# Performance work log

Measured on AMD Instinct MI355X. Metric: run time of the kernel, lower is better.

Reference implementation:

```python
import jax, jax.numpy as jnp
import numpy as np

NUM_HEADS = 16

def setup_inputs() -> dict:
    key = jax.random.key(0)
    kq, kk, kv = jax.random.split(key, 3)
    B, S, D = 4, 2048, 1024
    return {
        "queries": jax.random.normal(kq, (B, S, D), dtype=jnp.float32),
        "keys": jax.random.normal(kk, (B, S, D), dtype=jnp.float32),
        "values": jax.random.normal(kv, (B, S, D), dtype=jnp.float32),
    }

def _split_heads(x):
    # [B, S, D] -> [B, H, S, Dh]
    B, S, D = x.shape
    return x.reshape(B, S, NUM_HEADS, D // NUM_HEADS).transpose(0, 2, 1, 3)

def reference(queries, keys, values):
    q = _split_heads(queries)   # [B, H, S, Dh]
    k = _split_heads(keys)
    v = _split_heads(values)
    d_k = k.shape[-1]
    scale = 1.0 / jnp.sqrt(jnp.asarray(d_k, dtype=q.dtype))
    # [B, H, S, S] score matrix (materialized, as in the original bmm path)
    scores = jnp.einsum('bhqd,bhkd->bhqk', q, k) * scale
    weights = jax.nn.softmax(scores, axis=-1)
    out = jnp.einsum('bhqk,bhkd->bhqd', weights, v)  # [B, H, S, Dh]
    B, H, S, Dh = out.shape
    return out.transpose(0, 2, 1, 3).reshape(B, S, H * Dh)
```

## Files before the change

kernel.cpp:

```cpp
#include <hip/hip_runtime.h>
#include <hip/hip_bf16.h>
#include <math.h>

#define SEQ    2048
#define NH     16
#define DH     64
#define DMODEL 1024
#define KT     64
#define NT     (SEQ/KT)
#define KH_BYTES (4 * NH * SEQ * DH * 2)

typedef __bf16 bf16x8 __attribute__((ext_vector_type(8)));
typedef float  f32x4  __attribute__((ext_vector_type(4)));
typedef float  f32x16 __attribute__((ext_vector_type(16)));
typedef unsigned u32x2 __attribute__((ext_vector_type(2)));
typedef unsigned short u16x8 __attribute__((ext_vector_type(8)));
typedef __attribute__((address_space(3))) unsigned int        lds_u32_t;
typedef __attribute__((address_space(1))) const unsigned int  g_u32_t;

__device__ __forceinline__ ushort f2bf(float f) {
    union { __hip_bfloat16 h; ushort u; } z;
    z.h = __float2bfloat16(f);
    return z.u;
}

__device__ __forceinline__ unsigned pk2(float lo, float hi) {
    unsigned r;
    asm("v_cvt_pk_bf16_f32 %0, %1, %2" : "=v"(r) : "v"(lo), "v"(hi));
    return r;
}

__device__ __forceinline__ float fexp2(float x) {
#if __has_builtin(__builtin_amdgcn_exp2f)
    return __builtin_amdgcn_exp2f(x);
#else
    float r; asm("v_exp_f32 %0, %1\n\ts_nop 0" : "=v"(r) : "v"(x)); return r;
#endif
}

__device__ __forceinline__ void load16(const char* g, char* l) {
    __builtin_amdgcn_global_load_lds((g_u32_t*)g, (lds_u32_t*)l, 16, 0, 0);
}

__global__ __launch_bounds__(256)
void prep_kv(const float* __restrict__ K, const float* __restrict__ V,
             ushort* __restrict__ Kh, ushort* __restrict__ Vt) {
    __shared__ __attribute__((aligned(16))) unsigned T[64 * 32];
    int blk = blockIdx.x;
    int tid = threadIdx.x;
    int isV = blk >> 11;
    int tix = blk & 2047;
    int st = tix & 31, bh = tix >> 5;
    int b = bh >> 4, h = bh & 15;
    int s0 = st * 64;
    int sr  = tid >> 2;
    int seg = tid & 3;

    const float* ip = (isV ? V : K) + ((size_t)(b * SEQ + s0 + sr)) * DMODEL + h * DH + seg * 16;
    float4 f0 = ((const float4*)ip)[0];
    float4 f1 = ((const float4*)ip)[1];
    float4 f2 = ((const float4*)ip)[2];
    float4 f3 = ((const float4*)ip)[3];
    unsigned wv[8];
    wv[0] = pk2(f0.x, f0.y); wv[1] = pk2(f0.z, f0.w);
    wv[2] = pk2(f1.x, f1.y); wv[3] = pk2(f1.z, f1.w);
    wv[4] = pk2(f2.x, f2.y); wv[5] = pk2(f2.z, f2.w);
    wv[6] = pk2(f3.x, f3.y); wv[7] = pk2(f3.z, f3.w);

    if (!isV) {
        union { unsigned u[4]; u16x8 v; } a, c;
        a.u[0]=wv[0]; a.u[1]=wv[1]; a.u[2]=wv[2]; a.u[3]=wv[3];
        c.u[0]=wv[4]; c.u[1]=wv[5]; c.u[2]=wv[6]; c.u[3]=wv[7];
        ushort* op = Kh + ((size_t)bh * SEQ + s0 + sr) * DH + seg * 16;
        *(u16x8*)op = a.v;
        *(u16x8*)(op + 8) = c.v;
    } else {
        int key = sr & 31;
        #pragma unroll
        for (int j = 0; j < 8; ++j) {
            int pos = (seg * 8 + j) ^ key;
            T[sr * 32 + pos] = wv[j];
        }
        __syncthreads();
        int dr = sr;
        int sseg = seg;
        const char* TB = (const char*)T;
        u16x8 o0, o1;
        #pragma unroll
        for (int i = 0; i < 8; ++i) {
            int s = sseg * 16 + i;
            int off = s * 128 + ((((dr >> 1) ^ (s & 31)) << 2) | ((dr & 1) << 1));
            o0[i] = *(const ushort*)(TB + off);
        }
        #pragma unroll
        for (int i = 0; i < 8; ++i) {
            int s = sseg * 16 + 8 + i;
            int off = s * 128 + ((((dr >> 1) ^ (s & 31)) << 2) | ((dr & 1) << 1));
            o1[i] = *(const ushort*)(TB + off);
        }
        ushort* op = Vt + (size_t)bh * (SEQ * DH) + st * (64 * 64) + dr * 64 + sseg * 16;
        *(u16x8*)op = o0;
        *(u16x8*)(op + 8) = o1;
    }
}

__global__ __launch_bounds__(256, 2)
void mha_fwd32(const float* __restrict__ Q, const ushort* __restrict__ Kh,
               const ushort* __restrict__ Vt, float* __restrict__ Out) {
    int raw = blockIdx.x;
    int bid = (raw & 7) * 64 + (raw >> 3);
    int qt = bid & 7;
    int bh = bid >> 3;
    int b = bh >> 4, h = bh & 15;

    const int tid  = threadIdx.x;
    const int lane = tid & 63;
    const int w    = tid >> 6;
    const int l31  = lane & 31;
    const int lh   = lane >> 5;

    __shared__ __attribute__((aligned(16))) ushort Ks[2][KT * DH];
    __shared__ __attribute__((aligned(16))) ushort Vs[2][KT * DH];

    int o0  = tid * 16;
    int o1  = o0 + 4096;
    int so0 = o0 ^ (((o0 >> 7) & 7) << 4);
    int so1 = o1 ^ (((o1 >> 7) & 7) << 4);
    const char* khead = (const char*)Kh + (size_t)bh * (SEQ * DH * 2);
    const char* vhead = (const char*)Vt + (size_t)bh * (SEQ * DH * 2);
    const char* kg0 = khead + so0;
    const char* kg1 = khead + so1;
    const char* vg0 = vhead + so0;
    const char* vg1 = vhead + so1;

    const float QSCALE = 0.125f * 1.4426950408889634f;
    bf16x8 qf[2][4];
    #pragma unroll
    for (int q2 = 0; q2 < 2; ++q2) {
        int qrow = qt * 256 + w * 64 + q2 * 32 + l31;
        const float* qp = Q + ((size_t)b * SEQ + qrow) * DMODEL + h * DH + lh * 8;
        #pragma unroll
        for (int ks = 0; ks < 4; ++ks) {
            float4 fa = *(const float4*)(qp + ks * 16);
            float4 fb = *(const float4*)(qp + ks * 16 + 4);
            union { unsigned u[4]; bf16x8 v; } z;
            z.u[0] = pk2(fa.x * QSCALE, fa.y * QSCALE);
            z.u[1] = pk2(fa.z * QSCALE, fa.w * QSCALE);
            z.u[2] = pk2(fb.x * QSCALE, fb.y * QSCALE);
            z.u[3] = pk2(fb.z * QSCALE, fb.w * QSCALE);
            qf[q2][ks] = z.v;
        }
    }

    f32x16 zro;
    #pragma unroll
    for (int i = 0; i < 16; ++i) zro[i] = 0.f;
    bf16x8 onesf;
    {
        union { unsigned u[4]; bf16x8 v; } z;
        z.u[0] = 0x3F803F80u; z.u[1] = 0x3F803F80u;
        z.u[2] = 0x3F803F80u; z.u[3] = 0x3F803F80u;
        onesf = z.v;
    }

    f32x16 oacc[2][2];
    #pragma unroll
    for (int a = 0; a < 2; ++a)
        #pragma unroll
        for (int d = 0; d < 2; ++d)
            #pragma unroll
            for (int i = 0; i < 16; ++i) oacc[a][d][i] = 0.f;
    f32x16 lacc[2];
    #pragma unroll
    for (int a = 0; a < 2; ++a)
        #pragma unroll
        for (int i = 0; i < 16; ++i) lacc[a][i] = 0.f;

    int swz = (l31 & 7) << 4;
    int offRd[2][4];
    #pragma unroll
    for (int x = 0; x < 2; ++x)
        #pragma unroll
        for (int ks = 0; ks < 4; ++ks)
            offRd[x][ks] = (x * 32 + l31) * 128 + ((ks * 32 + lh * 16) ^ swz);

    {
        char* kb = (char*)&Ks[0][0] + w * 1024;
        char* vb = (char*)&Vs[0][0] + w * 1024;
        load16(kg0, kb); load16(kg1, kb + 4096);
        load16(vg0, vb); load16(vg1, vb + 4096);
        kg0 += KT * DH * 2; kg1 += KT * DH * 2; vg0 += KT * DH * 2; vg1 += KT * DH * 2;
    }
    __syncthreads();

    int buf = 0;
    for (int kt = 0; kt < NT; ++kt) {
        if (kt + 1 < NT) {
            char* kb = (char*)&Ks[buf ^ 1][0] + w * 1024;
            char* vb = (char*)&Vs[buf ^ 1][0] + w * 1024;
            load16(kg0, kb); load16(kg1, kb + 4096);
            load16(vg0, vb); load16(vg1, vb + 4096);
            kg0 += KT * DH * 2; kg1 += KT * DH * 2; vg0 += KT * DH * 2; vg1 += KT * DH * 2;
        }
        const char* kbb = (const char*)&Ks[buf][0];
        const char* vbb = (const char*)&Vs[buf][0];

        f32x16 sc[2][2];
        __builtin_amdgcn_s_setprio(1);
        #pragma unroll
        for (int t = 0; t < 2; ++t) {
            #pragma unroll
            for (int ks = 0; ks < 4; ++ks) {
                bf16x8 kf = *(const bf16x8*)(kbb + offRd[t][ks]);
                if (ks == 0) {
                    sc[0][t] = __builtin_amdgcn_mfma_f32_32x32x16_bf16(kf, qf[0][0], zro, 0, 0, 0);
                    sc[1][t] = __builtin_amdgcn_mfma_f32_32x32x16_bf16(kf, qf[1][0], zro, 0, 0, 0);
                } else {
                    sc[0][t] = __builtin_amdgcn_mfma_f32_32x32x16_bf16(kf, qf[0][ks], sc[0][t], 0, 0, 0);
                    sc[1][t] = __builtin_amdgcn_mfma_f32_32x32x16_bf16(kf, qf[1][ks], sc[1][t], 0, 0, 0);
                }
            }
        }
        __builtin_amdgcn_s_setprio(0);

        bf16x8 pa[2][4];
        #pragma unroll
        for (int q2 = 0; q2 < 2; ++q2) {
            float e[2][16];
            #pragma unroll
            for (int t = 0; t < 2; ++t)
                #pragma unroll
                for (int r = 0; r < 16; ++r)
                    e[t][r] = fexp2(sc[q2][t][r]);
            #pragma unroll
            for (int t = 0; t < 2; ++t) {
                #pragma unroll
                for (int s = 0; s < 2; ++s) {
                    unsigned X  = pk2(e[t][8 * s + 0], e[t][8 * s + 1]);
                    unsigned Bw = pk2(e[t][8 * s + 2], e[t][8 * s + 3]);
                    unsigned Y  = pk2(e[t][8 * s + 4], e[t][8 * s + 5]);
                    unsigned Dw = pk2(e[t][8 * s + 6], e[t][8 * s + 7]);
                    u32x2 pq = __builtin_amdgcn_permlane32_swap(X, Y, false, false);
                    u32x2 rs = __builtin_amdgcn_permlane32_swap(Bw, Dw, false, false);
                    union { unsigned u[4]; bf16x8 v; } z;
                    z.u[0] = pq.x; z.u[1] = rs.x; z.u[2] = pq.y; z.u[3] = rs.y;
                    pa[q2][2 * t + s] = z.v;
                }
            }
        }

        __builtin_amdgcn_s_setprio(1);
        #pragma unroll
        for (int dt = 0; dt < 2; ++dt) {
            #pragma unroll
            for (int ks = 0; ks < 4; ++ks) {
                bf16x8 vf = *(const bf16x8*)(vbb + offRd[dt][ks]);
                oacc[0][dt] = __builtin_amdgcn_mfma_f32_32x32x16_bf16(pa[0][ks], vf, oacc[0][dt], 0, 0, 0);
                oacc[1][dt] = __builtin_amdgcn_mfma_f32_32x32x16_bf16(pa[1][ks], vf, oacc[1][dt], 0, 0, 0);
            }
        }
        #pragma unroll
        for (int ks = 0; ks < 4; ++ks) {
            lacc[0] = __builtin_amdgcn_mfma_f32_32x32x16_bf16(pa[0][ks], onesf, lacc[0], 0, 0, 0);
            lacc[1] = __builtin_amdgcn_mfma_f32_32x32x16_bf16(pa[1][ks], onesf, lacc[1], 0, 0, 0);
        }
        __builtin_amdgcn_s_setprio(0);

        __syncthreads();
        buf ^= 1;
    }

    #pragma unroll
    for (int q2 = 0; q2 < 2; ++q2) {
        #pragma unroll
        for (int r = 0; r < 16; ++r) {
            float rl = __builtin_amdgcn_rcpf(lacc[q2][r]);
            int qp_ = (r & 3) + 8 * (r >> 2) + 4 * lh;
            int qrow = qt * 256 + w * 64 + q2 * 32 + qp_;
            float* op = Out + ((size_t)b * SEQ + qrow) * DMODEL + h * DH + l31;
            op[0]  = oacc[q2][0][r] * rl;
            op[32] = oacc[q2][1][r] * rl;
        }
    }
}

__global__ __launch_bounds__(256)
void mha_fwd_fallback(const float* __restrict__ Q, const float* __restrict__ K,
                      const float* __restrict__ V, float* __restrict__ Out) {
    int raw = blockIdx.x;
    int bid = (raw & 7) * 256 + (raw >> 3);
    int qt = bid & 31;
    int bh = bid >> 5;
    int b  = bh >> 4;
    int h  = bh & 15;
    const int tid  = threadIdx.x;
    const int lane = tid & 63;
    const int w    = tid >> 6;
    const int l15  = lane & 15;
    const int g    = lane >> 4;
    __shared__ ushort KsS[KT * DH];
    __shared__ ushort VTS[KT * DH];
    __shared__ ushort PlS[4][16 * KT];
    char* KsB = (char*)KsS;
    char* VTB = (char*)VTS;
    char* PlB = (char*)&PlS[w][0];
    const size_t base = ((size_t)b * SEQ) * DMODEL + (size_t)h * DH;
    const float QSCALE = 0.125f * 1.4426950408889634f;
    bf16x8 qa[2];
    {
        int qrow = qt * 64 + w * 16 + l15;
        const float* qp = Q + base + (size_t)qrow * DMODEL;
        for (int ds = 0; ds < 2; ++ds) {
            float4 f0 = *(const float4*)(qp + ds * 32 + g * 8);
            float4 f1 = *(const float4*)(qp + ds * 32 + g * 8 + 4);
            union { ushort u[8]; bf16x8 v; } pk;
            pk.u[0] = f2bf(f0.x * QSCALE); pk.u[1] = f2bf(f0.y * QSCALE);
            pk.u[2] = f2bf(f0.z * QSCALE); pk.u[3] = f2bf(f0.w * QSCALE);
            pk.u[4] = f2bf(f1.x * QSCALE); pk.u[5] = f2bf(f1.y * QSCALE);
            pk.u[6] = f2bf(f1.z * QSCALE); pk.u[7] = f2bf(f1.w * QSCALE);
            qa[ds] = pk.v;
        }
    }
    f32x4 oacc[4];
    for (int i = 0; i < 4; ++i) { oacc[i][0]=0.f; oacc[i][1]=0.f; oacc[i][2]=0.f; oacc[i][3]=0.f; }
    float m_r[4], l_r[4];
    for (int r = 0; r < 4; ++r) { m_r[r] = -3.0e38f; l_r[r] = 0.f; }
    for (int kt = 0; kt < SEQ / KT; ++kt) {
        const int kbase = kt * KT;
        for (int i = 0; i < 4; ++i) {
            int pos  = i * 256 + tid;
            int krow = pos >> 4;
            int d4   = (pos & 15) * 4;
            const float* kp = K + base + (size_t)(kbase + krow) * DMODEL + d4;
            float4 f = *(const float4*)kp;
            ushort4 u = make_ushort4(f2bf(f.x), f2bf(f.y), f2bf(f.z), f2bf(f.w));
            int off = (krow * 128 + d4 * 2) ^ ((krow & 7) << 4);
            *(ushort4*)(KsB + off) = u;
        }
        {
            int kg = tid >> 4;
            int d4 = (tid & 15) * 4;
            const float* vp = V + base + (size_t)(kbase + kg * 4) * DMODEL + d4;
            float4 r0 = *(const float4*)(vp);
            float4 r1 = *(const float4*)(vp + DMODEL);
            float4 r2 = *(const float4*)(vp + 2 * DMODEL);
            float4 r3 = *(const float4*)(vp + 3 * DMODEL);
            ushort4 c0 = make_ushort4(f2bf(r0.x), f2bf(r1.x), f2bf(r2.x), f2bf(r3.x));
            ushort4 c1 = make_ushort4(f2bf(r0.y), f2bf(r1.y), f2bf(r2.y), f2bf(r3.y));
            ushort4 c2 = make_ushort4(f2bf(r0.z), f2bf(r1.z), f2bf(r2.z), f2bf(r3.z));
            ushort4 c3 = make_ushort4(f2bf(r0.w), f2bf(r1.w), f2bf(r2.w), f2bf(r3.w));
            int row, off;
            row = d4 + 0; off = (row * 128 + kg * 8) ^ ((row & 7) << 4); *(ushort4*)(VTB + off) = c0;
            row = d4 + 1; off = (row * 128 + kg * 8) ^ ((row & 7) << 4); *(ushort4*)(VTB + off) = c1;
            row = d4 + 2; off = (row * 128 + kg * 8) ^ ((row & 7) << 4); *(ushort4*)(VTB + off) = c2;
            row = d4 + 3; off = (row * 128 + kg * 8) ^ ((row & 7) << 4); *(ushort4*)(VTB + off) = c3;
        }
        __syncthreads();
        f32x4 sc[4];
        for (int sub = 0; sub < 4; ++sub) {
            f32x4 a; a[0]=0.f; a[1]=0.f; a[2]=0.f; a[3]=0.f;
            for (int ds = 0; ds < 2; ++ds) {
                int krow = sub * 16 + l15;
                int off = (krow * 128 + ds * 64 + g * 16) ^ ((krow & 7) << 4);
                bf16x8 kb = *(const bf16x8*)(KsB + off);
                a = __builtin_amdgcn_mfma_f32_16x16x32_bf16(qa[ds], kb, a, 0, 0, 0);
            }
            sc[sub] = a;
        }
        float corr[4];
        float p[4][4];
        for (int r = 0; r < 4; ++r) {
            float t = fmaxf(fmaxf(sc[0][r], sc[1][r]), fmaxf(sc[2][r], sc[3][r]));
            t = fmaxf(t, __shfl_xor(t, 1));
            t = fmaxf(t, __shfl_xor(t, 2));
            t = fmaxf(t, __shfl_xor(t, 4));
            t = fmaxf(t, __shfl_xor(t, 8));
            float mn = fmaxf(m_r[r], t);
            corr[r] = exp2f(m_r[r] - mn);
            m_r[r] = mn;
            float s = 0.f;
            for (int sub = 0; sub < 4; ++sub) {
                float e = exp2f(sc[sub][r] - mn);
                p[sub][r] = e;
                s += e;
            }
            s += __shfl_xor(s, 1);
            s += __shfl_xor(s, 2);
            s += __shfl_xor(s, 4);
            s += __shfl_xor(s, 8);
            l_r[r] = l_r[r] * corr[r] + s;
        }
        for (int dsub = 0; dsub < 4; ++dsub)
            for (int r = 0; r < 4; ++r)
                oacc[dsub][r] *= corr[r];
        for (int r = 0; r < 4; ++r) {
            int row = g * 4 + r;
            for (int sub = 0; sub < 4; ++sub) {
                int off = (row * 128 + (sub * 16 + l15) * 2) ^ ((row & 7) << 4);
                *(ushort*)(PlB + off) = f2bf(p[sub][r]);
            }
        }
        bf16x8 pa[2];
        for (int ks = 0; ks < 2; ++ks) {
            int off = (l15 * 128 + ks * 64 + g * 16) ^ ((l15 & 7) << 4);
            pa[ks] = *(const bf16x8*)(PlB + off);
        }
        for (int dsub = 0; dsub < 4; ++dsub) {
            f32x4 a = oacc[dsub];
            for (int ks = 0; ks < 2; ++ks) {
                int row = dsub * 16 + l15;
                int off = (row * 128 + ks * 64 + g * 16) ^ ((row & 7) << 4);
                bf16x8 vb = *(const bf16x8*)(VTB + off);
                a = __builtin_amdgcn_mfma_f32_16x16x32_bf16(pa[ks], vb, a, 0, 0, 0);
            }
            oacc[dsub] = a;
        }
        __syncthreads();
    }
    for (int r = 0; r < 4; ++r) {
        float rl = 1.0f / l_r[r];
        int qrow = qt * 64 + w * 16 + g * 4 + r;
        float* op = Out + ((size_t)b * SEQ + qrow) * DMODEL + (size_t)h * DH;
        for (int dsub = 0; dsub < 4; ++dsub)
            op[dsub * 16 + l15] = oacc[dsub][r] * rl;
    }
}

extern "C" void kernel_launch(void* const* d_in, const int* in_sizes, int n_in,
                              void* d_out, int out_size, void* d_ws, size_t ws_size,
                              hipStream_t stream) {
    const float* Q = (const float*)d_in[0];
    const float* K = (const float*)d_in[1];
    const float* V = (const float*)d_in[2];
    float* Out = (float*)d_out;

    if (ws_size >= (size_t)2 * KH_BYTES) {
        ushort* Kh = (ushort*)d_ws;
        ushort* Vt = (ushort*)((char*)d_ws + KH_BYTES);
        prep_kv<<<dim3(4096), dim3(256), 0, stream>>>(K, V, Kh, Vt);
        mha_fwd32<<<dim3(512), dim3(256), 0, stream>>>(Q, Kh, Vt, Out);
    } else {
        mha_fwd_fallback<<<dim3(2048), dim3(256), 0, stream>>>(Q, K, V, Out);
    }
}
```

Measured before the change: 200.1 us.

## Drop LDS double-buffering and read K/V fragments directly from global memory

Removes the LDS staging buffers, the async global-to-LDS copies and the per-tile block barrier. Each wave now loads its K and V MFMA operands straight from global memory using unswizzled offsets, which map to the same elements as the old swizzled LDS reads. The aim is to cut barrier and LDS traffic overhead. In exchange, all four waves fetch the same tile redundantly through the cache hierarchy, and there is no explicit prefetch, so global-load latency may be exposed on every tile.

```diff
diff --git a/kernel.cpp b/kernel.cpp
--- a/kernel.cpp
+++ b/kernel.cpp
@@ -15,8 +15,6 @@
 typedef float  f32x16 __attribute__((ext_vector_type(16)));
 typedef unsigned u32x2 __attribute__((ext_vector_type(2)));
 typedef unsigned short u16x8 __attribute__((ext_vector_type(8)));
-typedef __attribute__((address_space(3))) unsigned int        lds_u32_t;
-typedef __attribute__((address_space(1))) const unsigned int  g_u32_t;
 
 __device__ __forceinline__ ushort f2bf(float f) {
     union { __hip_bfloat16 h; ushort u; } z;
@@ -36,10 +34,6 @@
 #else
     float r; asm("v_exp_f32 %0, %1\n\ts_nop 0" : "=v"(r) : "v"(x)); return r;
 #endif
-}
-
-__device__ __forceinline__ void load16(const char* g, char* l) {
-    __builtin_amdgcn_global_load_lds((g_u32_t*)g, (lds_u32_t*)l, 16, 0, 0);
 }
 
 __global__ __launch_bounds__(256)
@@ -119,19 +113,15 @@
     const int l31  = lane & 31;
     const int lh   = lane >> 5;
 
-    __shared__ __attribute__((aligned(16))) ushort Ks[2][KT * DH];
-    __shared__ __attribute__((aligned(16))) ushort Vs[2][KT * DH];
-
-    int o0  = tid * 16;
-    int o1  = o0 + 4096;
-    int so0 = o0 ^ (((o0 >> 7) & 7) << 4);
-    int so1 = o1 ^ (((o1 >> 7) & 7) << 4);
     const char* khead = (const char*)Kh + (size_t)bh * (SEQ * DH * 2);
     const char* vhead = (const char*)Vt + (size_t)bh * (SEQ * DH * 2);
-    const char* kg0 = khead + so0;
-    const char* kg1 = khead + so1;
-    const char* vg0 = vhead + so0;
-    const char* vg1 = vhead + so1;
+
+    int foff[2][4];
+    #pragma unroll
+    for (int x = 0; x < 2; ++x)
+        #pragma unroll
+        for (int ks = 0; ks < 4; ++ks)
+            foff[x][ks] = (x * 32 + l31) * 128 + ks * 32 + lh * 16;
 
     const float QSCALE = 0.125f * 1.4426950408889634f;
     bf16x8 qf[2][4];
@@ -176,34 +166,9 @@
         #pragma unroll
         for (int i = 0; i < 16; ++i) lacc[a][i] = 0.f;
 
-    int swz = (l31 & 7) << 4;
-    int offRd[2][4];
-    #pragma unroll
-    for (int x = 0; x < 2; ++x)
-        #pragma unroll
-        for (int ks = 0; ks < 4; ++ks)
-            offRd[x][ks] = (x * 32 + l31) * 128 + ((ks * 32 + lh * 16) ^ swz);
-
-    {
-        char* kb = (char*)&Ks[0][0] + w * 1024;
-        char* vb = (char*)&Vs[0][0] + w * 1024;
-        load16(kg0, kb); load16(kg1, kb + 4096);
-        load16(vg0, vb); load16(vg1, vb + 4096);
-        kg0 += KT * DH * 2; kg1 += KT * DH * 2; vg0 += KT * DH * 2; vg1 += KT * DH * 2;
-    }
-    __syncthreads();
-
-    int buf = 0;
     for (int kt = 0; kt < NT; ++kt) {
-        if (kt + 1 < NT) {
-            char* kb = (char*)&Ks[buf ^ 1][0] + w * 1024;
-            char* vb = (char*)&Vs[buf ^ 1][0] + w * 1024;
-            load16(kg0, kb); load16(kg1, kb + 4096);
-            load16(vg0, vb); load16(vg1, vb + 4096);
-            kg0 += KT * DH * 2; kg1 += KT * DH * 2; vg0 += KT * DH * 2; vg1 += KT * DH * 2;
-        }
-        const char* kbb = (const char*)&Ks[buf][0];
-        const char* vbb = (const char*)&Vs[buf][0];
+        const char* ktile = khead + (size_t)kt * 8192;
+        const char* vtile = vhead + (size_t)kt * 8192;
 
         f32x16 sc[2][2];
         __builtin_amdgcn_s_setprio(1);
@@ -211,7 +176,7 @@
         for (int t = 0; t < 2; ++t) {
             #pragma unroll
             for (int ks = 0; ks < 4; ++ks) {
-                bf16x8 kf = *(const bf16x8*)(kbb + offRd[t][ks]);
+                bf16x8 kf = *(const bf16x8*)(ktile + foff[t][ks]);
                 if (ks == 0) {
                     sc[0][t] = __builtin_amdgcn_mfma_f32_32x32x16_bf16(kf, qf[0][0], zro, 0, 0, 0);
                     sc[1][t] = __builtin_amdgcn_mfma_f32_32x32x16_bf16(kf, qf[1][0], zro, 0, 0, 0);
@@ -222,6 +187,13 @@
             }
         }
         __builtin_amdgcn_s_setprio(0);
+
+        bf16x8 vf[2][4];
+        #pragma unroll
+        for (int dt = 0; dt < 2; ++dt)
+            #pragma unroll
+            for (int ks = 0; ks < 4; ++ks)
+                vf[dt][ks] = *(const bf16x8*)(vtile + foff[dt][ks]);
 
         bf16x8 pa[2][4];
         #pragma unroll
@@ -254,9 +226,8 @@
         for (int dt = 0; dt < 2; ++dt) {
             #pragma unroll
             for (int ks = 0; ks < 4; ++ks) {
-                bf16x8 vf = *(const bf16x8*)(vbb + offRd[dt][ks]);
-                oacc[0][dt] = __builtin_amdgcn_mfma_f32_32x32x16_bf16(pa[0][ks], vf, oacc[0][dt], 0, 0, 0);
-                oacc[1][dt] = __builtin_amdgcn_mfma_f32_32x32x16_bf16(pa[1][ks], vf, oacc[1][dt], 0, 0, 0);
+                oacc[0][dt] = __builtin_amdgcn_mfma_f32_32x32x16_bf16(pa[0][ks], vf[dt][ks], oacc[0][dt], 0, 0, 0);
+                oacc[1][dt] = __builtin_amdgcn_mfma_f32_32x32x16_bf16(pa[1][ks], vf[dt][ks], oacc[1][dt], 0, 0, 0);
             }
         }
         #pragma unroll
@@ -265,9 +236,6 @@
             lacc[1] = __builtin_amdgcn_mfma_f32_32x32x16_bf16(pa[1][ks], onesf, lacc[1], 0, 0, 0);
         }
         __builtin_amdgcn_s_setprio(0);
-
-        __syncthreads();
-        buf ^= 1;
     }
 
     #pragma unroll
```

Result: slower. 260.7 us (+30.3%).
